# Performance work log

Hardware: AMD Instinct MI355X
Metric: run time of the kernel (lower is better)

## Reference

```python
import jax, jax.numpy as jnp
import numpy as np

EP = 65536      # entity pairs (segments)
L = 8           # rows per span
N = EP * L      # total logit rows
C = 97          # relation classes (class 0 = threshold class)
BIG = 1e30


def setup_inputs() -> dict:
    key = jax.random.key(0)
    k1, k2 = jax.random.split(key)
    logits = jax.random.normal(k1, (N, C), dtype=jnp.float32)
    labels = (jax.random.uniform(k2, (EP, C)) < 0.03).astype(jnp.float32)
    starts = jnp.arange(EP, dtype=jnp.int32) * L
    pos = jnp.stack([starts, starts + L], axis=1)  # contiguous [st, en) spans
    return {"logits": logits, "labels": labels, "pos": pos}


def reference(logits, labels, pos):
    ep = pos.shape[0]
    n = logits.shape[0]
    # contiguous spans cover [0, N): row i belongs to segment j with end_j > i
    seg_ids = jnp.searchsorted(pos[:, 1], jnp.arange(n, dtype=pos.dtype), side="right")
    # ragged per-span max-reduction (single fused segment-max)
    e_logits = jax.ops.segment_max(logits, seg_ids, num_segments=ep)  # [EP, C]
    # threshold column taken from the first ep rows of raw logits
    e_logits = e_logits.at[:, 0].set(logits[:ep, 0])

    th_label = jnp.zeros_like(labels).at[:, 0].set(1.0)
    labels = labels.at[:, 0].set(0.0)
    p_mask = labels + th_label
    n_mask = 1.0 - labels

    loss1 = -(jax.nn.log_softmax(e_logits - (1.0 - p_mask) * BIG, axis=-1) * labels).sum(1)
    loss2 = -(jax.nn.log_softmax(e_logits - (1.0 - n_mask) * BIG, axis=-1) * th_label).sum(1)
    return (loss1 + loss2).mean()
```

## Files before the change

kernel.cpp:

```cpp
#include <hip/hip_runtime.h>
#include <math.h>

#define EP 65536
#define C 97
#define L 8
#define WAVES 4
#define ITERS 8
#define SEG_PER_BLOCK (WAVES * ITERS)
#define NBLOCKS (EP / SEG_PER_BLOCK)
#define SEG_FLOATS (L * C)

typedef float f4 __attribute__((ext_vector_type(4)));

template <int CTRL, int RMASK>
__device__ __forceinline__ float dpp_step(float v) {
    return v + __int_as_float(__builtin_amdgcn_update_dpp(
                   0, __float_as_int(v), CTRL, RMASK, 0xf, true));
}

__device__ __forceinline__ void dpp_wsum2(float& a, float& b) {
    a = dpp_step<0x128, 0xf>(a); b = dpp_step<0x128, 0xf>(b);
    a = dpp_step<0x124, 0xf>(a); b = dpp_step<0x124, 0xf>(b);
    a = dpp_step<0x122, 0xf>(a); b = dpp_step<0x122, 0xf>(b);
    a = dpp_step<0x121, 0xf>(a); b = dpp_step<0x121, 0xf>(b);
    a = dpp_step<0x142, 0xa>(a); b = dpp_step<0x142, 0xa>(b);
    a = dpp_step<0x143, 0xc>(a); b = dpp_step<0x143, 0xc>(b);
    a = __int_as_float(__builtin_amdgcn_readlane(__float_as_int(a), 63));
    b = __int_as_float(__builtin_amdgcn_readlane(__float_as_int(b), 63));
}
__device__ __forceinline__ float dpp_wsum(float v) {
    v = dpp_step<0x128, 0xf>(v);
    v = dpp_step<0x124, 0xf>(v);
    v = dpp_step<0x122, 0xf>(v);
    v = dpp_step<0x121, 0xf>(v);
    v = dpp_step<0x142, 0xa>(v);
    v = dpp_step<0x143, 0xc>(v);
    return __int_as_float(__builtin_amdgcn_readlane(__float_as_int(v), 63));
}

__global__ __launch_bounds__(256) void atloss_main(
        const float* __restrict__ logits,
        const float* __restrict__ labels,
        const int*   __restrict__ pos,
        float*       __restrict__ partials) {
    const int tid  = threadIdx.x;
    const int w    = tid >> 6;
    const int lane = tid & 63;
    const int jbase = blockIdx.x * SEG_PER_BLOCK + w * ITERS;

    __shared__ float s_log[WAVES * SEG_FLOATS];
    __shared__ float s_loss[WAVES];
    float* seg_s = s_log + w * SEG_FLOATS;
    f4*    s4    = (f4*)seg_s;

    const int  c0   = lane;
    const int  c1   = lane + 64;
    const bool has1 = (c1 < C);

    int st_l = 0;
    if (lane < ITERS) st_l = pos[2 * (jbase + lane)];
    int st_s[ITERS];
#pragma unroll
    for (int k = 0; k < ITERS; ++k)
        st_s[k] = __builtin_amdgcn_readlane(st_l, k);

    const f4* g4 = (const f4*)(logits + (size_t)st_s[0] * C);
    f4 A0 = __builtin_nontemporal_load(g4 + lane);
    f4 A1 = __builtin_nontemporal_load(g4 + lane + 64);
    f4 A2 = __builtin_nontemporal_load(g4 + lane + 128);
    f4 A3 = (f4){0.f, 0.f, 0.f, 0.f};
    if (lane < 2) A3 = __builtin_nontemporal_load(g4 + 192 + lane);
    const size_t lbb = (size_t)jbase * C;
    float LB0 = __builtin_nontemporal_load(labels + lbb + c0);
    float LB1 = has1 ? __builtin_nontemporal_load(labels + lbb + c1) : 0.0f;
    float ETH = logits[(size_t)jbase * C];

    float acc_uni = 0.0f, acc_spos = 0.0f;

#pragma unroll
    for (int it = 0; it < ITERS; ++it) {
        const f4 B0 = A0, B1 = A1, B2 = A2, B3 = A3;
        const float lb0 = LB0, lb1 = LB1, eth = ETH;
        if (it + 1 < ITERS) {
            const int j1 = jbase + it + 1;
            const f4* g4n = (const f4*)(logits + (size_t)st_s[it + 1] * C);
            A0 = __builtin_nontemporal_load(g4n + lane);
            A1 = __builtin_nontemporal_load(g4n + lane + 64);
            A2 = __builtin_nontemporal_load(g4n + lane + 128);
            if (lane < 2) A3 = __builtin_nontemporal_load(g4n + 192 + lane);
            const size_t lbn = (size_t)j1 * C;
            LB0 = __builtin_nontemporal_load(labels + lbn + c0);
            LB1 = has1 ? __builtin_nontemporal_load(labels + lbn + c1) : 0.0f;
            ETH = logits[(size_t)j1 * C];
        }

        s4[lane] = B0; s4[lane + 64] = B1; s4[lane + 128] = B2;
        if (lane < 2) s4[192 + lane] = B3;

        float e0, e1 = -INFINITY;
        {
            const float m01 = fmaxf(seg_s[0 * C + c0], seg_s[1 * C + c0]);
            const float m23 = fmaxf(seg_s[2 * C + c0], seg_s[3 * C + c0]);
            const float m45 = fmaxf(seg_s[4 * C + c0], seg_s[5 * C + c0]);
            const float m67 = fmaxf(seg_s[6 * C + c0], seg_s[7 * C + c0]);
            e0 = fmaxf(fmaxf(m01, m23), fmaxf(m45, m67));
        }
        if (has1) {
            const float m01 = fmaxf(seg_s[0 * C + c1], seg_s[1 * C + c1]);
            const float m23 = fmaxf(seg_s[2 * C + c1], seg_s[3 * C + c1]);
            const float m45 = fmaxf(seg_s[4 * C + c1], seg_s[5 * C + c1]);
            const float m67 = fmaxf(seg_s[6 * C + c1], seg_s[7 * C + c1]);
            e1 = fmaxf(fmaxf(m01, m23), fmaxf(m45, m67));
        }
        if (lane == 0) e0 = eth;

        const bool p0 = (lane > 0) && (lb0 > 0.5f);
        const bool p1 = has1 && (lb1 > 0.5f);
        const float npos = (float)(__popcll(__ballot(p0)) +
                                   __popcll(__ballot(p1)));

        const float x0 = __expf(e0);
        const float x1 = has1 ? __expf(e1) : 0.0f;

        float s_all  = x0 + x1;
        float sp_pos = (p0 ? x0 : 0.0f) + (p1 ? x1 : 0.0f);
        dpp_wsum2(s_all, sp_pos);

        const float sp = __expf(eth) + sp_pos;
        const float sn = s_all - sp_pos;
        acc_uni  += npos * __logf(sp) + (__logf(sn) - eth);
        acc_spos += (p0 ? e0 : 0.0f) + (p1 ? e1 : 0.0f);
    }

    const float wloss = acc_uni - dpp_wsum(acc_spos);

    if (lane == 0) s_loss[w] = wloss;
    __syncthreads();
    if (tid == 0) {
        partials[blockIdx.x] = s_loss[0] + s_loss[1] + s_loss[2] + s_loss[3];
    }
}

__global__ __launch_bounds__(256) void atloss_reduce(
        const float* __restrict__ partials, int n, float* __restrict__ out) {
    __shared__ double sh[256];
    double acc = 0.0;
    for (int i = threadIdx.x; i < n; i += 256) acc += (double)partials[i];
    sh[threadIdx.x] = acc;
    __syncthreads();
    for (int s = 128; s > 0; s >>= 1) {
        if (threadIdx.x < s) sh[threadIdx.x] += sh[threadIdx.x + s];
        __syncthreads();
    }
    if (threadIdx.x == 0) out[0] = (float)(sh[0] / (double)EP);
}

extern "C" void kernel_launch(void* const* d_in, const int* in_sizes, int n_in,
                              void* d_out, int out_size, void* d_ws, size_t ws_size,
                              hipStream_t stream) {
    const float* logits = (const float*)d_in[0];
    const float* labels = (const float*)d_in[1];
    const int*   pos    = (const int*)d_in[2];
    float* out      = (float*)d_out;
    float* partials = (float*)d_ws;

    atloss_main<<<NBLOCKS, 256, 0, stream>>>(logits, labels, pos, partials);
    atloss_reduce<<<1, 256, 0, stream>>>(partials, NBLOCKS, out);
}
```

Measured before the change: 46.58 us.

## Deepen logits prefetch to two segments and hoist label/threshold loads upfront

```diff
diff --git a/kernel.cpp b/kernel.cpp
--- a/kernel.cpp
+++ b/kernel.cpp
@@ -11,13 +11,13 @@
 #define SEG_FLOATS (L * C)
 
 typedef float f4 __attribute__((ext_vector_type(4)));
+#define NT(p) __builtin_nontemporal_load(p)
 
 template <int CTRL, int RMASK>
 __device__ __forceinline__ float dpp_step(float v) {
     return v + __int_as_float(__builtin_amdgcn_update_dpp(
                    0, __float_as_int(v), CTRL, RMASK, 0xf, true));
 }
-
 __device__ __forceinline__ void dpp_wsum2(float& a, float& b) {
     a = dpp_step<0x128, 0xf>(a); b = dpp_step<0x128, 0xf>(b);
     a = dpp_step<0x124, 0xf>(a); b = dpp_step<0x124, 0xf>(b);
@@ -64,73 +64,85 @@
     for (int k = 0; k < ITERS; ++k)
         st_s[k] = __builtin_amdgcn_readlane(st_l, k);
 
-    const f4* g4 = (const f4*)(logits + (size_t)st_s[0] * C);
-    f4 A0 = __builtin_nontemporal_load(g4 + lane);
-    f4 A1 = __builtin_nontemporal_load(g4 + lane + 64);
-    f4 A2 = __builtin_nontemporal_load(g4 + lane + 128);
-    f4 A3 = (f4){0.f, 0.f, 0.f, 0.f};
-    if (lane < 2) A3 = __builtin_nontemporal_load(g4 + 192 + lane);
-    const size_t lbb = (size_t)jbase * C;
-    float LB0 = __builtin_nontemporal_load(labels + lbb + c0);
-    float LB1 = has1 ? __builtin_nontemporal_load(labels + lbb + c1) : 0.0f;
-    float ETH = logits[(size_t)jbase * C];
+    unsigned pm0 = 0, pm1 = 0;
+#pragma unroll
+    for (int k = 0; k < ITERS; ++k) {
+        const size_t lb = (size_t)(jbase + k) * C;
+        const float l0 = NT(labels + lb + c0);
+        const float l1 = has1 ? NT(labels + lb + c1) : 0.0f;
+        pm0 |= ((lane > 0) && (l0 > 0.5f)) ? (1u << k) : 0u;
+        pm1 |= (has1 && (l1 > 0.5f)) ? (1u << k) : 0u;
+    }
+    float eth_s[ITERS];
+#pragma unroll
+    for (int k = 0; k < ITERS; ++k)
+        eth_s[k] = __int_as_float(__builtin_amdgcn_readfirstlane(
+            __float_as_int(logits[(size_t)(jbase + k) * C])));
+
+    f4 A0, A1, A2, A3 = (f4){0.f, 0.f, 0.f, 0.f};
+    f4 B0, B1, B2, B3 = (f4){0.f, 0.f, 0.f, 0.f};
+    {
+        const f4* ga = (const f4*)(logits + (size_t)st_s[0] * C);
+        A0 = NT(ga + lane); A1 = NT(ga + lane + 64); A2 = NT(ga + lane + 128);
+        if (lane < 2) A3 = NT(ga + 192 + lane);
+        const f4* gb = (const f4*)(logits + (size_t)st_s[1] * C);
+        B0 = NT(gb + lane); B1 = NT(gb + lane + 64); B2 = NT(gb + lane + 128);
+        if (lane < 2) B3 = NT(gb + 192 + lane);
+    }
 
     float acc_uni = 0.0f, acc_spos = 0.0f;
 
-#pragma unroll
-    for (int it = 0; it < ITERS; ++it) {
-        const f4 B0 = A0, B1 = A1, B2 = A2, B3 = A3;
-        const float lb0 = LB0, lb1 = LB1, eth = ETH;
-        if (it + 1 < ITERS) {
-            const int j1 = jbase + it + 1;
-            const f4* g4n = (const f4*)(logits + (size_t)st_s[it + 1] * C);
-            A0 = __builtin_nontemporal_load(g4n + lane);
-            A1 = __builtin_nontemporal_load(g4n + lane + 64);
-            A2 = __builtin_nontemporal_load(g4n + lane + 128);
-            if (lane < 2) A3 = __builtin_nontemporal_load(g4n + 192 + lane);
-            const size_t lbn = (size_t)j1 * C;
-            LB0 = __builtin_nontemporal_load(labels + lbn + c0);
-            LB1 = has1 ? __builtin_nontemporal_load(labels + lbn + c1) : 0.0f;
-            ETH = logits[(size_t)j1 * C];
-        }
+#define PROCESS(R0, R1, R2, R3, IT)                                          \
+    {                                                                        \
+        s4[lane] = R0; s4[lane + 64] = R1; s4[lane + 128] = R2;              \
+        if (lane < 2) s4[192 + lane] = R3;                                   \
+        if ((IT) + 2 < ITERS) {                                              \
+            const f4* gn = (const f4*)(logits + (size_t)st_s[(IT) + 2] * C); \
+            R0 = NT(gn + lane); R1 = NT(gn + lane + 64);                     \
+            R2 = NT(gn + lane + 128);                                        \
+            if (lane < 2) R3 = NT(gn + 192 + lane);                          \
+        }                                                                    \
+        const float eth = eth_s[(IT)];                                       \
+        float e0, e1 = -INFINITY;                                            \
+        {                                                                    \
+            const float m01 = fmaxf(seg_s[0 * C + c0], seg_s[1 * C + c0]);   \
+            const float m23 = fmaxf(seg_s[2 * C + c0], seg_s[3 * C + c0]);   \
+            const float m45 = fmaxf(seg_s[4 * C + c0], seg_s[5 * C + c0]);   \
+            const float m67 = fmaxf(seg_s[6 * C + c0], seg_s[7 * C + c0]);   \
+            e0 = fmaxf(fmaxf(m01, m23), fmaxf(m45, m67));                    \
+        }                                                                    \
+        if (has1) {                                                          \
+            const float m01 = fmaxf(seg_s[0 * C + c1], seg_s[1 * C + c1]);   \
+            const float m23 = fmaxf(seg_s[2 * C + c1], seg_s[3 * C + c1]);   \
+            const float m45 = fmaxf(seg_s[4 * C + c1], seg_s[5 * C + c1]);   \
+            const float m67 = fmaxf(seg_s[6 * C + c1], seg_s[7 * C + c1]);   \
+            e1 = fmaxf(fmaxf(m01, m23), fmaxf(m45, m67));                    \
+        }                                                                    \
+        if (lane == 0) e0 = eth;                                             \
+        const bool p0 = (pm0 >> (IT)) & 1u;                                  \
+        const bool p1 = (pm1 >> (IT)) & 1u;                                  \
+        const float npos = (float)(__popcll(__ballot(p0)) +                  \
+                                   __popcll(__ballot(p1)));                  \
+        const float x0 = __expf(e0);                                         \
+        const float x1 = has1 ? __expf(e1) : 0.0f;                           \
+        float s_all  = x0 + x1;                                              \
+        float sp_pos = (p0 ? x0 : 0.0f) + (p1 ? x1 : 0.0f);                  \
+        dpp_wsum2(s_all, sp_pos);                                            \
+        const float sp = __expf(eth) + sp_pos;                               \
+        const float sn = s_all - sp_pos;                                     \
+        acc_uni  += npos * __logf(sp) + (__logf(sn) - eth);                  \
+        acc_spos += (p0 ? e0 : 0.0f) + (p1 ? e1 : 0.0f);                     \
+    }
 
-        s4[lane] = B0; s4[lane + 64] = B1; s4[lane + 128] = B2;
-        if (lane < 2) s4[192 + lane] = B3;
-
-        float e0, e1 = -INFINITY;
-        {
-            const float m01 = fmaxf(seg_s[0 * C + c0], seg_s[1 * C + c0]);
-            const float m23 = fmaxf(seg_s[2 * C + c0], seg_s[3 * C + c0]);
-            const float m45 = fmaxf(seg_s[4 * C + c0], seg_s[5 * C + c0]);
-            const float m67 = fmaxf(seg_s[6 * C + c0], seg_s[7 * C + c0]);
-            e0 = fmaxf(fmaxf(m01, m23), fmaxf(m45, m67));
-        }
-        if (has1) {
-            const float m01 = fmaxf(seg_s[0 * C + c1], seg_s[1 * C + c1]);
-            const float m23 = fmaxf(seg_s[2 * C + c1], seg_s[3 * C + c1]);
-            const float m45 = fmaxf(seg_s[4 * C + c1], seg_s[5 * C + c1]);
-            const float m67 = fmaxf(seg_s[6 * C + c1], seg_s[7 * C + c1]);
-            e1 = fmaxf(fmaxf(m01, m23), fmaxf(m45, m67));
-        }
-        if (lane == 0) e0 = eth;
-
-        const bool p0 = (lane > 0) && (lb0 > 0.5f);
-        const bool p1 = has1 && (lb1 > 0.5f);
-        const float npos = (float)(__popcll(__ballot(p0)) +
-                                   __popcll(__ballot(p1)));
-
-        const float x0 = __expf(e0);
-        const float x1 = has1 ? __expf(e1) : 0.0f;
-
-        float s_all  = x0 + x1;
-        float sp_pos = (p0 ? x0 : 0.0f) + (p1 ? x1 : 0.0f);
-        dpp_wsum2(s_all, sp_pos);
-
-        const float sp = __expf(eth) + sp_pos;
-        const float sn = s_all - sp_pos;
-        acc_uni  += npos * __logf(sp) + (__logf(sn) - eth);
-        acc_spos += (p0 ? e0 : 0.0f) + (p1 ? e1 : 0.0f);
-    }
+    PROCESS(A0, A1, A2, A3, 0)
+    PROCESS(B0, B1, B2, B3, 1)
+    PROCESS(A0, A1, A2, A3, 2)
+    PROCESS(B0, B1, B2, B3, 3)
+    PROCESS(A0, A1, A2, A3, 4)
+    PROCESS(B0, B1, B2, B3, 5)
+    PROCESS(A0, A1, A2, A3, 6)
+    PROCESS(B0, B1, B2, B3, 7)
+#undef PROCESS
 
     const float wloss = acc_uni - dpp_wsum(acc_spos);
 
```

After: 46.72 us. About the same (+0.3%).
